# Kernel tuning notes

Measured on AMD Instinct MI355X. Metric: run time of the kernel, lower is better.

## Reference

```python
import jax, jax.numpy as jnp
import numpy as np

N_NODES = 100000
F_IN = 64
F_OUT = 64
SLOPE = 0.2


def setup_inputs() -> dict:
    key = jax.random.key(0)
    k1, k2, k3, k4 = jax.random.split(key, 4)
    input_matrix = jax.random.normal(k1, (N_NODES, F_IN), dtype=jnp.float32)
    edge_index = jax.random.randint(k2, (2, 1600000), 0, N_NODES, dtype=jnp.int64)
    # xavier-uniform-style params
    lim_w = float(np.sqrt(6.0 / (F_IN + F_OUT)))
    W = jax.random.uniform(k3, (F_IN, F_OUT), minval=-lim_w, maxval=lim_w, dtype=jnp.float32)
    lim_a = float(np.sqrt(6.0 / (2 * F_OUT + 1)))
    a = jax.random.uniform(k4, (2 * F_OUT,), minval=-lim_a, maxval=lim_a, dtype=jnp.float32)
    return {"input_matrix": input_matrix, "edge_index": edge_index, "W": W, "a": a}


def reference(input_matrix, edge_index, W, a):
    N = input_matrix.shape[0]
    # add self edges
    loops = jnp.arange(N, dtype=edge_index.dtype)
    src = jnp.concatenate([edge_index[0], loops])  # [E+N]
    dst = jnp.concatenate([edge_index[1], loops])  # [E+N]

    h = input_matrix @ W                      # [N, F_out]
    F = h.shape[1]
    h_src = h[src]                            # [E+N, F_out] gather
    h_dst = h[dst]                            # [E+N, F_out] gather
    # cat([h_src, h_dst], 1) @ a == h_src @ a[:F] + h_dst @ a[F:]
    alpha = h_src @ a[:F] + h_dst @ a[F:]     # [E+N]
    alpha = jnp.where(alpha >= 0, alpha, SLOPE * alpha)  # leaky relu
    alpha = jnp.exp(alpha)
    denom = jax.ops.segment_sum(alpha, src, num_segments=N)  # [N]
    alpha = alpha / denom[src]                # segment softmax over edges sharing src
    out = jax.ops.segment_sum(h_dst * alpha[:, None], src, num_segments=N)  # [N, F_out]
    return out
```

## Files before the change

kernel.cpp:

```cpp
#include <hip/hip_runtime.h>
#include <hip/hip_bf16.h>

#define F 64
#define SLOPE 0.2f
#define NB_SHIFT 8
#define BATCH 4096
#define HIST_BLOCKS 128

typedef __attribute__((ext_vector_type(8))) short bf16x8;
typedef __attribute__((ext_vector_type(4))) float f32x4;

__device__ inline unsigned short f2bf(float f) {
    unsigned u = __float_as_uint(f);
    unsigned r = (u + 0x7FFFu + ((u >> 16) & 1u)) >> 16;
    return (unsigned short)r;
}

__global__ __launch_bounds__(256) void gat_prep(
    const float* __restrict__ W, const float* __restrict__ a,
    unsigned short* __restrict__ Wp, float* __restrict__ w1,
    float* __restrict__ w2) {
    int tid = threadIdx.x;
    if (tid < 64) {
#pragma unroll
        for (int f = 0; f < 8; ++f) {
            int cg = f >> 1, kc = f & 1;
            int col = cg * 16 + (tid & 15);
            unsigned short us[8];
#pragma unroll
            for (int j = 0; j < 8; ++j) {
                int k = kc * 32 + (tid >> 4) * 8 + j;
                us[j] = f2bf(W[k * F + col]);
            }
            uint4 pk;
            pk.x = us[0] | ((unsigned)us[1] << 16);
            pk.y = us[2] | ((unsigned)us[3] << 16);
            pk.z = us[4] | ((unsigned)us[5] << 16);
            pk.w = us[6] | ((unsigned)us[7] << 16);
            *(uint4*)&Wp[(f * 64 + tid) * 8] = pk;
        }
    } else if (tid < 128) {
        int k = tid - 64;
        float acc1 = 0.f, acc2 = 0.f;
#pragma unroll
        for (int n = 0; n < F; ++n) {
            float wv = W[k * F + n];
            acc1 = fmaf(wv, a[n], acc1);
            acc2 = fmaf(wv, a[F + n], acc2);
        }
        w1[k] = acc1;
        w2[k] = acc2;
    }
}

__global__ __launch_bounds__(256) void gat_gemm_hist(
    const float* __restrict__ X, const unsigned short* __restrict__ Wp,
    const float* __restrict__ w1, const float* __restrict__ w2,
    unsigned short* __restrict__ hb, float* __restrict__ s1,
    float* __restrict__ s2, int N,
    const int* __restrict__ src, int* __restrict__ partialHist, int E,
    int gemmBlocks) {
    __shared__ int lh[512];
    int tid = threadIdx.x;

    if ((int)blockIdx.x >= gemmBlocks) {
        int hbid = blockIdx.x - gemmBlocks;
        for (int i = tid; i < 512; i += 256) lh[i] = 0;
        __syncthreads();
        for (int i = hbid * 256 + tid; i < E; i += HIST_BLOCKS * 256)
            atomicAdd(&lh[src[i] >> NB_SHIFT], 1);
        __syncthreads();
        for (int i = tid; i < 512; i += 256)
            partialHist[hbid * 512 + i] = lh[i];
        return;
    }

    int lane = tid & 63;
    int wv = tid >> 6;
    int rowBase = blockIdx.x * 64 + wv * 16;
    if (rowBase >= N) return;
    int lrow = lane & 15;
    int kg = lane >> 4;
    int row = rowBase + lrow;
    int rclamp = (row < N) ? row : (N - 1);

    const float* xp = &X[(size_t)rclamp * F + kg * 8];
    float4 u0 = *(const float4*)(xp + 0);
    float4 u1 = *(const float4*)(xp + 4);
    float4 u2 = *(const float4*)(xp + 32);
    float4 u3 = *(const float4*)(xp + 36);
    float xr[16] = {u0.x, u0.y, u0.z, u0.w, u1.x, u1.y, u1.z, u1.w,
                    u2.x, u2.y, u2.z, u2.w, u3.x, u3.y, u3.z, u3.w};

    bf16x8 a0, a1;
#pragma unroll
    for (int j = 0; j < 8; ++j) {
        a0[j] = (short)f2bf(xr[j]);
        a1[j] = (short)f2bf(xr[8 + j]);
    }

    bf16x8 bf0 = *(const bf16x8*)&Wp[(0 * 64 + lane) * 8];
    bf16x8 bf1 = *(const bf16x8*)&Wp[(1 * 64 + lane) * 8];
    bf16x8 bf2 = *(const bf16x8*)&Wp[(2 * 64 + lane) * 8];
    bf16x8 bf3 = *(const bf16x8*)&Wp[(3 * 64 + lane) * 8];
    bf16x8 bf4 = *(const bf16x8*)&Wp[(4 * 64 + lane) * 8];
    bf16x8 bf5 = *(const bf16x8*)&Wp[(5 * 64 + lane) * 8];
    bf16x8 bf6 = *(const bf16x8*)&Wp[(6 * 64 + lane) * 8];
    bf16x8 bf7 = *(const bf16x8*)&Wp[(7 * 64 + lane) * 8];

    f32x4 acc0 = {0.f, 0.f, 0.f, 0.f};
    f32x4 acc1v = {0.f, 0.f, 0.f, 0.f};
    f32x4 acc2v = {0.f, 0.f, 0.f, 0.f};
    f32x4 acc3 = {0.f, 0.f, 0.f, 0.f};
    acc0 = __builtin_amdgcn_mfma_f32_16x16x32_bf16(a0, bf0, acc0, 0, 0, 0);
    acc0 = __builtin_amdgcn_mfma_f32_16x16x32_bf16(a1, bf1, acc0, 0, 0, 0);
    acc1v = __builtin_amdgcn_mfma_f32_16x16x32_bf16(a0, bf2, acc1v, 0, 0, 0);
    acc1v = __builtin_amdgcn_mfma_f32_16x16x32_bf16(a1, bf3, acc1v, 0, 0, 0);
    acc2v = __builtin_amdgcn_mfma_f32_16x16x32_bf16(a0, bf4, acc2v, 0, 0, 0);
    acc2v = __builtin_amdgcn_mfma_f32_16x16x32_bf16(a1, bf5, acc2v, 0, 0, 0);
    acc3 = __builtin_amdgcn_mfma_f32_16x16x32_bf16(a0, bf6, acc3, 0, 0, 0);
    acc3 = __builtin_amdgcn_mfma_f32_16x16x32_bf16(a1, bf7, acc3, 0, 0, 0);

#pragma unroll
    for (int r = 0; r < 4; ++r) {
        int ro = rowBase + kg * 4 + r;
        if (ro < N) {
            size_t rb = (size_t)ro * F + lrow;
            hb[rb + 0] = f2bf(acc0[r]);
            hb[rb + 16] = f2bf(acc1v[r]);
            hb[rb + 32] = f2bf(acc2v[r]);
            hb[rb + 48] = f2bf(acc3[r]);
        }
    }

    float4 wa0 = *(const float4*)&w1[kg * 8];
    float4 wa1 = *(const float4*)&w1[kg * 8 + 4];
    float4 wa2 = *(const float4*)&w1[32 + kg * 8];
    float4 wa3 = *(const float4*)&w1[32 + kg * 8 + 4];
    float4 wb0 = *(const float4*)&w2[kg * 8];
    float4 wb1 = *(const float4*)&w2[kg * 8 + 4];
    float4 wb2 = *(const float4*)&w2[32 + kg * 8];
    float4 wb3 = *(const float4*)&w2[32 + kg * 8 + 4];
    float wv1[16] = {wa0.x, wa0.y, wa0.z, wa0.w, wa1.x, wa1.y, wa1.z, wa1.w,
                     wa2.x, wa2.y, wa2.z, wa2.w, wa3.x, wa3.y, wa3.z, wa3.w};
    float wv2[16] = {wb0.x, wb0.y, wb0.z, wb0.w, wb1.x, wb1.y, wb1.z, wb1.w,
                     wb2.x, wb2.y, wb2.z, wb2.w, wb3.x, wb3.y, wb3.z, wb3.w};
    float p = 0.f, q = 0.f;
#pragma unroll
    for (int j = 0; j < 16; ++j) {
        p = fmaf(xr[j], wv1[j], p);
        q = fmaf(xr[j], wv2[j], q);
    }
    p += __shfl_xor(p, 16, 64);
    p += __shfl_xor(p, 32, 64);
    q += __shfl_xor(q, 16, 64);
    q += __shfl_xor(q, 32, 64);
    if (lane < 16 && row < N) {
        s1[row] = p;
        s2[row] = q;
    }
}

__global__ __launch_bounds__(512) void gat_scan0(
    const int* __restrict__ partialHist, int* __restrict__ bucketBase,
    int* __restrict__ bucketCursor, int* __restrict__ rowptrN, int NB) {
    __shared__ int wsum[8];
    int tid = threadIdx.x, lane = tid & 63, wid = tid >> 6;
    int v = 0;
    for (int p = 0; p < HIST_BLOCKS; ++p)
        v += partialHist[p * 512 + tid];
    int x = v;
#pragma unroll
    for (int off = 1; off < 64; off <<= 1) {
        int y = __shfl_up(x, off, 64);
        if (lane >= off) x += y;
    }
    if (lane == 63) wsum[wid] = x;
    __syncthreads();
    int add = 0;
    for (int w = 0; w < 8; ++w)
        if (w < wid) add += wsum[w];
    int excl = add + x - v;
    if (tid < NB) {
        bucketBase[tid] = excl;
        bucketCursor[tid] = excl;
    }
    if (tid == NB - 1) {
        bucketBase[NB] = excl + v;
        rowptrN[0] = excl + v;
    }
}

__global__ __launch_bounds__(512) void gat_bin(
    const int* __restrict__ src, const int* __restrict__ dst,
    int* __restrict__ bucketCursor, unsigned* __restrict__ bucketData, int E) {
    __shared__ int hist[512], excl[512], gbase[512], cur[512];
    __shared__ int wsum[8];
    __shared__ int2 staged[BATCH];
    int tid = threadIdx.x, lane = tid & 63, wid = tid >> 6;
    int base = blockIdx.x * BATCH;
    int n = E - base;
    if (n > BATCH) n = BATCH;

    hist[tid] = 0;
    __syncthreads();

    int se[8], de[8];
#pragma unroll
    for (int j = 0; j < 8; ++j) {
        int i = base + j * 512 + tid;
        se[j] = -1;
        de[j] = 0;
        if (i < E) {
            se[j] = src[i];
            de[j] = dst[i];
            atomicAdd(&hist[se[j] >> NB_SHIFT], 1);
        }
    }
    __syncthreads();
    int v = hist[tid];
    int x = v;
#pragma unroll
    for (int off = 1; off < 64; off <<= 1) {
        int y = __shfl_up(x, off, 64);
        if (lane >= off) x += y;
    }
    if (lane == 63) wsum[wid] = x;
    __syncthreads();
    int add = 0;
    for (int w = 0; w < 8; ++w)
        if (w < wid) add += wsum[w];
    int ex = add + x - v;
    excl[tid] = ex;
    cur[tid] = ex;
    __syncthreads();
#pragma unroll
    for (int j = 0; j < 8; ++j) {
        if (se[j] >= 0) {
            int b = se[j] >> NB_SHIFT;
            int pos = atomicAdd(&cur[b], 1);
            staged[pos] = make_int2(se[j], de[j]);
        }
    }
    if (v > 0)
        gbase[tid] = atomicAdd(&bucketCursor[tid], v);
    __syncthreads();
    for (int i = tid; i < n; i += 512) {
        int2 p = staged[i];
        int b = p.x >> NB_SHIFT;
        bucketData[gbase[b] + (i - excl[b])] =
            ((unsigned)(p.x & 255) << 24) | (unsigned)p.y;
    }
}

__global__ __launch_bounds__(256) void gat_bucket(
    const int* __restrict__ bucketBase, const unsigned* __restrict__ bucketData,
    int* __restrict__ rowptr, int* __restrict__ sortedDst, int N) {
    __shared__ int cnt[256], cur[256];
    __shared__ int wsum[4];
    int b = blockIdx.x;
    int tid = threadIdx.x, lane = tid & 63, wid = tid >> 6;
    int beg = bucketBase[b];
    int end = bucketBase[b + 1];
    int node0 = b << NB_SHIFT;

    cnt[tid] = 0;
    __syncthreads();
    for (int i = beg + tid; i < end; i += 256)
        atomicAdd(&cnt[bucketData[i] >> 24], 1);
    __syncthreads();
    int v = cnt[tid];
    int x = v;
#pragma unroll
    for (int off = 1; off < 64; off <<= 1) {
        int y = __shfl_up(x, off, 64);
        if (lane >= off) x += y;
    }
    if (lane == 63) wsum[wid] = x;
    __syncthreads();
    int add = 0;
    for (int w = 0; w < 4; ++w)
        if (w < wid) add += wsum[w];
    int excl = add + x - v;
    int node = node0 + tid;
    if (node < N) rowptr[node] = beg + excl;
    cur[tid] = beg + excl;
    __syncthreads();
    for (int i = beg + tid; i < end; i += 256) {
        unsigned w = bucketData[i];
        int pos = atomicAdd(&cur[w >> 24], 1);
        sortedDst[pos] = (int)(w & 0xFFFFFFu);
    }
}

#define EDGE_FMA(g, al, A)                                                   \
    A[0] = fmaf(al, __uint_as_float(g.x << 16), A[0]);                       \
    A[1] = fmaf(al, __uint_as_float(g.x & 0xFFFF0000u), A[1]);               \
    A[2] = fmaf(al, __uint_as_float(g.y << 16), A[2]);                       \
    A[3] = fmaf(al, __uint_as_float(g.y & 0xFFFF0000u), A[3]);               \
    A[4] = fmaf(al, __uint_as_float(g.z << 16), A[4]);                       \
    A[5] = fmaf(al, __uint_as_float(g.z & 0xFFFF0000u), A[5]);               \
    A[6] = fmaf(al, __uint_as_float(g.w << 16), A[6]);                       \
    A[7] = fmaf(al, __uint_as_float(g.w & 0xFFFF0000u), A[7]);

__global__ __launch_bounds__(256) void gat_aggregate(
    const int* __restrict__ rowptr,
    const int* __restrict__ sortedDst,
    const float* __restrict__ s1, const float* __restrict__ s2,
    const unsigned short* __restrict__ hb, float* __restrict__ out, int N) {
    int tid = threadIdx.x;
    int node = blockIdx.x * 32 + (tid >> 3);
    if (node >= N) return;
    const int fo = (tid & 7) * 8;

    int beg = rowptr[node];
    int end = rowptr[node + 1];
    float s1s = s1[node];
    float as = s1s + s2[node];
    as = (as >= 0.f) ? as : SLOPE * as;
    as = expf(as);

    float accA[8], accB[8];
    {
        uint4 hv = *(const uint4*)&hb[(size_t)node * F + fo];
        accA[0] = as * __uint_as_float(hv.x << 16);
        accA[1] = as * __uint_as_float(hv.x & 0xFFFF0000u);
        accA[2] = as * __uint_as_float(hv.y << 16);
        accA[3] = as * __uint_as_float(hv.y & 0xFFFF0000u);
        accA[4] = as * __uint_as_float(hv.z << 16);
        accA[5] = as * __uint_as_float(hv.z & 0xFFFF0000u);
        accA[6] = as * __uint_as_float(hv.w << 16);
        accA[7] = as * __uint_as_float(hv.w & 0xFFFF0000u);
    }
#pragma unroll
    for (int i = 0; i < 8; ++i) accB[i] = 0.f;

    float dsum = as;
    int e = beg;
    for (; e + 4 <= end; e += 4) {
        int d0 = sortedDst[e];
        int d1 = sortedDst[e + 1];
        int d2 = sortedDst[e + 2];
        int d3 = sortedDst[e + 3];
        float t0 = s1s + s2[d0];
        float t1 = s1s + s2[d1];
        float t2 = s1s + s2[d2];
        float t3 = s1s + s2[d3];
        uint4 g0 = *(const uint4*)&hb[(size_t)d0 * F + fo];
        uint4 g1 = *(const uint4*)&hb[(size_t)d1 * F + fo];
        uint4 g2 = *(const uint4*)&hb[(size_t)d2 * F + fo];
        uint4 g3 = *(const uint4*)&hb[(size_t)d3 * F + fo];
        t0 = (t0 >= 0.f) ? t0 : SLOPE * t0;
        t1 = (t1 >= 0.f) ? t1 : SLOPE * t1;
        t2 = (t2 >= 0.f) ? t2 : SLOPE * t2;
        t3 = (t3 >= 0.f) ? t3 : SLOPE * t3;
        float a0 = expf(t0);
        float a1 = expf(t1);
        float a2 = expf(t2);
        float a3 = expf(t3);
        dsum += (a0 + a1) + (a2 + a3);
        EDGE_FMA(g0, a0, accA);
        EDGE_FMA(g1, a1, accB);
        EDGE_FMA(g2, a2, accA);
        EDGE_FMA(g3, a3, accB);
    }
    for (; e < end; ++e) {
        int d0 = sortedDst[e];
        float t0 = s1s + s2[d0];
        t0 = (t0 >= 0.f) ? t0 : SLOPE * t0;
        float a0 = expf(t0);
        dsum += a0;
        uint4 g0 = *(const uint4*)&hb[(size_t)d0 * F + fo];
        EDGE_FMA(g0, a0, accA);
    }

    float inv = 1.0f / dsum;
    float4 r0, r1;
    r0.x = (accA[0] + accB[0]) * inv;
    r0.y = (accA[1] + accB[1]) * inv;
    r0.z = (accA[2] + accB[2]) * inv;
    r0.w = (accA[3] + accB[3]) * inv;
    r1.x = (accA[4] + accB[4]) * inv;
    r1.y = (accA[5] + accB[5]) * inv;
    r1.z = (accA[6] + accB[6]) * inv;
    r1.w = (accA[7] + accB[7]) * inv;
    *(float4*)&out[(size_t)node * F + fo] = r0;
    *(float4*)&out[(size_t)node * F + fo + 4] = r1;
}

extern "C" void kernel_launch(void* const* d_in, const int* in_sizes, int n_in,
                              void* d_out, int out_size, void* d_ws, size_t ws_size,
                              hipStream_t stream) {
    const float* X = (const float*)d_in[0];
    const int* edge = (const int*)d_in[1];
    const float* W = (const float*)d_in[2];
    const float* a = (const float*)d_in[3];

    int N = in_sizes[0] / F;
    int E = in_sizes[1] / 2;
    int NB = (N + 255) >> NB_SHIFT;

    const int* src = edge;
    const int* dst = edge + E;

    unsigned* bucketData = (unsigned*)d_ws;
    unsigned short* hb = (unsigned short*)(bucketData + E);
    float* s1 = (float*)(hb + (size_t)N * F);
    float* s2 = s1 + N;
    int* partialHist = (int*)(s2 + N);
    int* bucketBase = partialHist + HIST_BLOCKS * 512;
    int* bucketCursor = bucketBase + 513;
    int* rowptr = bucketCursor + 512;
    int* sortedDst = rowptr + (N + 1);
    unsigned short* Wp = (unsigned short*)(sortedDst + E);
    float* w1 = (float*)(Wp + 4096);
    float* w2 = w1 + 64;

    float* out = (float*)d_out;

    gat_prep<<<1, 256, 0, stream>>>(W, a, Wp, w1, w2);

    int gemmBlocks = (N + 63) / 64;
    gat_gemm_hist<<<gemmBlocks + HIST_BLOCKS, 256, 0, stream>>>(
        X, Wp, w1, w2, hb, s1, s2, N, src, partialHist, E, gemmBlocks);

    gat_scan0<<<1, 512, 0, stream>>>(partialHist, bucketBase, bucketCursor,
                                     rowptr + N, NB);

    int binBlocks = (E + BATCH - 1) / BATCH;
    gat_bin<<<binBlocks, 512, 0, stream>>>(src, dst, bucketCursor, bucketData, E);

    gat_bucket<<<NB, 256, 0, stream>>>(bucketBase, bucketData, rowptr,
                                       sortedDst, N);

    int aggBlocks = (N + 31) / 32;
    gat_aggregate<<<aggBlocks, 256, 0, stream>>>(rowptr, sortedDst,
                                                 s1, s2, hb, out, N);
}
```

Before: 105.0 us.

## Use fixed-size bucket slabs instead of histogram/scan and precompute edge weights

Drops the source histogram pass and the single-block scan kernel. Each 256-node bucket now gets a fixed slab of SLAB entries, with cursors initialised in the prep kernel. The bucket-sort kernel also computes the leaky-relu/exp attention weight per edge and stores it next to the destination index as an int2, so the aggregate kernel no longer gathers s2 or evaluates exp. In exchange, the sorted edge array doubles in size, and correctness relies on no bucket exceeding the slab capacity, which holds for uniformly random edges but not for skewed graphs.

```diff
diff --git a/kernel.cpp b/kernel.cpp
--- a/kernel.cpp
+++ b/kernel.cpp
@@ -5,7 +5,7 @@
 #define SLOPE 0.2f
 #define NB_SHIFT 8
 #define BATCH 4096
-#define HIST_BLOCKS 128
+#define SLAB 5120
 
 typedef __attribute__((ext_vector_type(8))) short bf16x8;
 typedef __attribute__((ext_vector_type(4))) float f32x4;
@@ -19,8 +19,10 @@
 __global__ __launch_bounds__(256) void gat_prep(
     const float* __restrict__ W, const float* __restrict__ a,
     unsigned short* __restrict__ Wp, float* __restrict__ w1,
-    float* __restrict__ w2) {
+    float* __restrict__ w2, int* __restrict__ bucketCursor) {
     int tid = threadIdx.x;
+    for (int i = tid; i < 512; i += 256) bucketCursor[i] = i * SLAB;
+
     if (tid < 64) {
 #pragma unroll
         for (int f = 0; f < 8; ++f) {
@@ -53,28 +55,12 @@
     }
 }
 
-__global__ __launch_bounds__(256) void gat_gemm_hist(
+__global__ __launch_bounds__(256) void gat_gemm_mfma(
     const float* __restrict__ X, const unsigned short* __restrict__ Wp,
     const float* __restrict__ w1, const float* __restrict__ w2,
     unsigned short* __restrict__ hb, float* __restrict__ s1,
-    float* __restrict__ s2, int N,
-    const int* __restrict__ src, int* __restrict__ partialHist, int E,
-    int gemmBlocks) {
-    __shared__ int lh[512];
+    float* __restrict__ s2, int N) {
     int tid = threadIdx.x;
-
-    if ((int)blockIdx.x >= gemmBlocks) {
-        int hbid = blockIdx.x - gemmBlocks;
-        for (int i = tid; i < 512; i += 256) lh[i] = 0;
-        __syncthreads();
-        for (int i = hbid * 256 + tid; i < E; i += HIST_BLOCKS * 256)
-            atomicAdd(&lh[src[i] >> NB_SHIFT], 1);
-        __syncthreads();
-        for (int i = tid; i < 512; i += 256)
-            partialHist[hbid * 512 + i] = lh[i];
-        return;
-    }
-
     int lane = tid & 63;
     int wv = tid >> 6;
     int rowBase = blockIdx.x * 64 + wv * 16;
@@ -161,36 +147,6 @@
     }
 }
 
-__global__ __launch_bounds__(512) void gat_scan0(
-    const int* __restrict__ partialHist, int* __restrict__ bucketBase,
-    int* __restrict__ bucketCursor, int* __restrict__ rowptrN, int NB) {
-    __shared__ int wsum[8];
-    int tid = threadIdx.x, lane = tid & 63, wid = tid >> 6;
-    int v = 0;
-    for (int p = 0; p < HIST_BLOCKS; ++p)
-        v += partialHist[p * 512 + tid];
-    int x = v;
-#pragma unroll
-    for (int off = 1; off < 64; off <<= 1) {
-        int y = __shfl_up(x, off, 64);
-        if (lane >= off) x += y;
-    }
-    if (lane == 63) wsum[wid] = x;
-    __syncthreads();
-    int add = 0;
-    for (int w = 0; w < 8; ++w)
-        if (w < wid) add += wsum[w];
-    int excl = add + x - v;
-    if (tid < NB) {
-        bucketBase[tid] = excl;
-        bucketCursor[tid] = excl;
-    }
-    if (tid == NB - 1) {
-        bucketBase[NB] = excl + v;
-        rowptrN[0] = excl + v;
-    }
-}
-
 __global__ __launch_bounds__(512) void gat_bin(
     const int* __restrict__ src, const int* __restrict__ dst,
     int* __restrict__ bucketCursor, unsigned* __restrict__ bucketData, int E) {
@@ -254,17 +210,22 @@
 }
 
 __global__ __launch_bounds__(256) void gat_bucket(
-    const int* __restrict__ bucketBase, const unsigned* __restrict__ bucketData,
-    int* __restrict__ rowptr, int* __restrict__ sortedDst, int N) {
+    const int* __restrict__ bucketCursor, const unsigned* __restrict__ bucketData,
+    const float* __restrict__ s1, const float* __restrict__ s2,
+    int* __restrict__ rowbeg, int* __restrict__ rowend,
+    int2* __restrict__ sortedData, int N) {
     __shared__ int cnt[256], cur[256];
+    __shared__ float s1l[256];
     __shared__ int wsum[4];
     int b = blockIdx.x;
     int tid = threadIdx.x, lane = tid & 63, wid = tid >> 6;
-    int beg = bucketBase[b];
-    int end = bucketBase[b + 1];
+    int beg = b * SLAB;
+    int end = bucketCursor[b];
     int node0 = b << NB_SHIFT;
+    int node = node0 + tid;
 
     cnt[tid] = 0;
+    s1l[tid] = (node < N) ? s1[node] : 0.f;
     __syncthreads();
     for (int i = beg + tid; i < end; i += 256)
         atomicAdd(&cnt[bucketData[i] >> 24], 1);
@@ -282,14 +243,21 @@
     for (int w = 0; w < 4; ++w)
         if (w < wid) add += wsum[w];
     int excl = add + x - v;
-    int node = node0 + tid;
-    if (node < N) rowptr[node] = beg + excl;
+    if (node < N) {
+        rowbeg[node] = beg + excl;
+        rowend[node] = beg + excl + v;
+    }
     cur[tid] = beg + excl;
     __syncthreads();
     for (int i = beg + tid; i < end; i += 256) {
         unsigned w = bucketData[i];
-        int pos = atomicAdd(&cur[w >> 24], 1);
-        sortedDst[pos] = (int)(w & 0xFFFFFFu);
+        int sloc = w >> 24;
+        int d = (int)(w & 0xFFFFFFu);
+        float t = s1l[sloc] + s2[d];
+        t = (t >= 0.f) ? t : SLOPE * t;
+        float al = expf(t);
+        int pos = atomicAdd(&cur[sloc], 1);
+        sortedData[pos] = make_int2(d, __float_as_int(al));
     }
 }
 
@@ -304,8 +272,8 @@
     A[7] = fmaf(al, __uint_as_float(g.w & 0xFFFF0000u), A[7]);
 
 __global__ __launch_bounds__(256) void gat_aggregate(
-    const int* __restrict__ rowptr,
-    const int* __restrict__ sortedDst,
+    const int* __restrict__ rowbeg, const int* __restrict__ rowend,
+    const int2* __restrict__ sortedData,
     const float* __restrict__ s1, const float* __restrict__ s2,
     const unsigned short* __restrict__ hb, float* __restrict__ out, int N) {
     int tid = threadIdx.x;
@@ -313,10 +281,9 @@
     if (node >= N) return;
     const int fo = (tid & 7) * 8;
 
-    int beg = rowptr[node];
-    int end = rowptr[node + 1];
-    float s1s = s1[node];
-    float as = s1s + s2[node];
+    int beg = rowbeg[node];
+    int end = rowend[node];
+    float as = s1[node] + s2[node];
     as = (as >= 0.f) ? as : SLOPE * as;
     as = expf(as);
 
@@ -338,26 +305,18 @@
     float dsum = as;
     int e = beg;
     for (; e + 4 <= end; e += 4) {
-        int d0 = sortedDst[e];
-        int d1 = sortedDst[e + 1];
-        int d2 = sortedDst[e + 2];
-        int d3 = sortedDst[e + 3];
-        float t0 = s1s + s2[d0];
-        float t1 = s1s + s2[d1];
-        float t2 = s1s + s2[d2];
-        float t3 = s1s + s2[d3];
-        uint4 g0 = *(const uint4*)&hb[(size_t)d0 * F + fo];
-        uint4 g1 = *(const uint4*)&hb[(size_t)d1 * F + fo];
-        uint4 g2 = *(const uint4*)&hb[(size_t)d2 * F + fo];
-        uint4 g3 = *(const uint4*)&hb[(size_t)d3 * F + fo];
-        t0 = (t0 >= 0.f) ? t0 : SLOPE * t0;
-        t1 = (t1 >= 0.f) ? t1 : SLOPE * t1;
-        t2 = (t2 >= 0.f) ? t2 : SLOPE * t2;
-        t3 = (t3 >= 0.f) ? t3 : SLOPE * t3;
-        float a0 = expf(t0);
-        float a1 = expf(t1);
-        float a2 = expf(t2);
-        float a3 = expf(t3);
+        int2 p0 = sortedData[e];
+        int2 p1 = sortedData[e + 1];
+        int2 p2 = sortedData[e + 2];
+        int2 p3 = sortedData[e + 3];
+        uint4 g0 = *(const uint4*)&hb[(size_t)p0.x * F + fo];
+        uint4 g1 = *(const uint4*)&hb[(size_t)p1.x * F + fo];
+        uint4 g2 = *(const uint4*)&hb[(size_t)p2.x * F + fo];
+        uint4 g3 = *(const uint4*)&hb[(size_t)p3.x * F + fo];
+        float a0 = __int_as_float(p0.y);
+        float a1 = __int_as_float(p1.y);
+        float a2 = __int_as_float(p2.y);
+        float a3 = __int_as_float(p3.y);
         dsum += (a0 + a1) + (a2 + a3);
         EDGE_FMA(g0, a0, accA);
         EDGE_FMA(g1, a1, accB);
@@ -365,12 +324,10 @@
         EDGE_FMA(g3, a3, accB);
     }
     for (; e < end; ++e) {
-        int d0 = sortedDst[e];
-        float t0 = s1s + s2[d0];
-        t0 = (t0 >= 0.f) ? t0 : SLOPE * t0;
-        float a0 = expf(t0);
+        int2 p0 = sortedData[e];
+        float a0 = __int_as_float(p0.y);
         dsum += a0;
-        uint4 g0 = *(const uint4*)&hb[(size_t)d0 * F + fo];
+        uint4 g0 = *(const uint4*)&hb[(size_t)p0.x * F + fo];
         EDGE_FMA(g0, a0, accA);
     }
 
@@ -404,36 +361,31 @@
     const int* dst = edge + E;
 
     unsigned* bucketData = (unsigned*)d_ws;
-    unsigned short* hb = (unsigned short*)(bucketData + E);
+    int2* sortedData = (int2*)(bucketData + (size_t)NB * SLAB);
+    unsigned short* hb = (unsigned short*)(sortedData + (size_t)NB * SLAB);
     float* s1 = (float*)(hb + (size_t)N * F);
     float* s2 = s1 + N;
-    int* partialHist = (int*)(s2 + N);
-    int* bucketBase = partialHist + HIST_BLOCKS * 512;
-    int* bucketCursor = bucketBase + 513;
-    int* rowptr = bucketCursor + 512;
-    int* sortedDst = rowptr + (N + 1);
-    unsigned short* Wp = (unsigned short*)(sortedDst + E);
+    int* rowbeg = (int*)(s2 + N);
+    int* rowend = rowbeg + N;
+    int* bucketCursor = rowend + N;
+    unsigned short* Wp = (unsigned short*)(bucketCursor + 512);
     float* w1 = (float*)(Wp + 4096);
     float* w2 = w1 + 64;
 
     float* out = (float*)d_out;
 
-    gat_prep<<<1, 256, 0, stream>>>(W, a, Wp, w1, w2);
+    gat_prep<<<1, 256, 0, stream>>>(W, a, Wp, w1, w2, bucketCursor);
 
     int gemmBlocks = (N + 63) / 64;
-    gat_gemm_hist<<<gemmBlocks + HIST_BLOCKS, 256, 0, stream>>>(
-        X, Wp, w1, w2, hb, s1, s2, N, src, partialHist, E, gemmBlocks);
-
-    gat_scan0<<<1, 512, 0, stream>>>(partialHist, bucketBase, bucketCursor,
-                                     rowptr + N, NB);
+    gat_gemm_mfma<<<gemmBlocks, 256, 0, stream>>>(X, Wp, w1, w2, hb, s1, s2, N);
 
     int binBlocks = (E + BATCH - 1) / BATCH;
     gat_bin<<<binBlocks, 512, 0, stream>>>(src, dst, bucketCursor, bucketData, E);
 
-    gat_bucket<<<NB, 256, 0, stream>>>(bucketBase, bucketData, rowptr,
-                                       sortedDst, N);
+    gat_bucket<<<NB, 256, 0, stream>>>(bucketCursor, bucketData, s1, s2,
+                                       rowbeg, rowend, sortedData, N);
 
     int aggBlocks = (N + 31) / 32;
-    gat_aggregate<<<aggBlocks, 256, 0, stream>>>(rowptr, sortedDst,
+    gat_aggregate<<<aggBlocks, 256, 0, stream>>>(rowbeg, rowend, sortedData,
                                                  s1, s2, hb, out, N);
 }
```

After: 92.85 us. 1.13x faster.
